# Optimization experiments

Hardware: AMD Instinct MI355X
Metric: run time of the kernel (lower is better)

The kernel has to match this reference:

```python
import jax, jax.numpy as jnp
import numpy as np

C = 512
K = 3
DIL = 1
EPS = 1e-6


def weight_quant(w):
    # BitNet b1.58 ternary quantization with straight-through estimator:
    # scale = mean(|w|); w_q = clamp(round(w/scale), -1, 1) * scale
    s = jnp.maximum(jnp.mean(jnp.abs(w)), 1e-5)
    q = jnp.clip(jnp.round(w / s), -1.0, 1.0) * s
    return w + jax.lax.stop_gradient(q - w)


def conv1d(x, w, b, padding, dilation):
    # x: [B, C, L], w: [O, I, K]
    y = jax.lax.conv_general_dilated(
        x, w, window_strides=(1,), padding=[(padding, padding)],
        rhs_dilation=(dilation,), dimension_numbers=("NCH", "OIH", "NCH"))
    return y + b[None, :, None]


def setup_inputs() -> dict:
    key = jax.random.key(0)
    k0, k1, k2, k3, k4 = jax.random.split(key, 5)
    fan_in = C * K
    lim = 1.0 / np.sqrt(fan_in)
    x = jax.random.normal(k0, (16, C, 4096), dtype=jnp.float32)
    w1 = jax.random.uniform(k1, (C, C, K), jnp.float32, -lim, lim)
    b1 = jax.random.uniform(k2, (C,), jnp.float32, -lim, lim)
    w2 = jax.random.uniform(k3, (C, C, K), jnp.float32, -lim, lim)
    b2 = jax.random.uniform(k4, (C,), jnp.float32, -lim, lim)
    g = jnp.ones((C,), dtype=jnp.float32)  # RMSNorm gain
    return {"x": x, "w1": w1, "b1": b1, "w2": w2, "b2": b2, "g": g}


def reference(x, w1, b1, w2, b2, g):
    residual = x
    # RMSNorm over channel axis (original transposes to [B,L,C], norms last dim)
    ms = jnp.mean(jnp.square(x), axis=1, keepdims=True)
    h = x * jax.lax.rsqrt(ms + EPS) * g[None, :, None]
    h = jax.nn.silu(h)
    p1 = (K * DIL - DIL) // 2
    h = conv1d(h, weight_quant(w1), b1, p1, DIL)
    h = jax.nn.silu(h)
    h = conv1d(h, weight_quant(w2), b2, K // 2, 1)
    return h + residual
```

## Files before the change

### kernel.cpp

```cpp
#include <hip/hip_runtime.h>

#define BATCH 16
#define CCH 512
#define LEN 4096
#define LPAD 4098

typedef unsigned short u16;
typedef __bf16 bf16x8 __attribute__((ext_vector_type(8)));
typedef float f32x4 __attribute__((ext_vector_type(4)));
typedef u16 u16x8 __attribute__((ext_vector_type(8)));
typedef u16 u16x4 __attribute__((ext_vector_type(4)));

__device__ __forceinline__ u16 f2bf(float f) {
    unsigned u = __float_as_uint(f);
    u = (u + 0x7fffu + ((u >> 16) & 1u)) >> 16;
    return (u16)u;
}
__device__ __forceinline__ float bf2f(u16 v) {
    return __uint_as_float(((unsigned)v) << 16);
}
__device__ __forceinline__ float silu_f(float v) {
    return v / (1.f + __expf(-v));
}
__device__ __forceinline__ void async16(const u16* g, u16* l) {
    __builtin_amdgcn_global_load_lds(
        (const __attribute__((address_space(1))) unsigned int*)g,
        (__attribute__((address_space(3))) unsigned int*)l, 16, 0, 0);
}

#define SBAR() __builtin_amdgcn_sched_barrier(0)
#define HWBAR() { SBAR(); __builtin_amdgcn_s_barrier(); SBAR(); }
#define WAIT_LGKM0() { asm volatile("s_waitcnt lgkmcnt(0)" ::: "memory"); SBAR(); }
#define WAIT_VM(n) { asm volatile("s_waitcnt vmcnt(" #n ")" ::: "memory"); SBAR(); }

__global__ __launch_bounds__(256)
void absmean_partial(const float* __restrict__ w1, const float* __restrict__ w2,
                     float* __restrict__ part) {
    const int tid = threadIdx.x;
    const int base = blockIdx.x * 3072;
    float s1 = 0.f, s2 = 0.f;
    for (int i = tid; i < 3072; i += 256) {
        s1 += fabsf(w1[base + i]);
        s2 += fabsf(w2[base + i]);
    }
    __shared__ float r1[256], r2[256];
    r1[tid] = s1; r2[tid] = s2;
    __syncthreads();
    for (int off = 128; off > 0; off >>= 1) {
        if (tid < off) { r1[tid] += r1[tid + off]; r2[tid] += r2[tid + off]; }
        __syncthreads();
    }
    if (tid == 0) { part[blockIdx.x] = r1[0]; part[256 + blockIdx.x] = r2[0]; }
}

__global__ __launch_bounds__(256)
void finalize_scale(const float* __restrict__ part, float* __restrict__ sv) {
    const int tid = threadIdx.x;
    __shared__ float r1[256], r2[256];
    r1[tid] = part[tid]; r2[tid] = part[256 + tid];
    __syncthreads();
    for (int off = 128; off > 0; off >>= 1) {
        if (tid < off) { r1[tid] += r1[tid + off]; r2[tid] += r2[tid + off]; }
        __syncthreads();
    }
    if (tid == 0) {
        sv[0] = fmaxf(r1[0] * (1.f / 786432.f), 1e-5f);
        sv[1] = fmaxf(r2[0] * (1.f / 786432.f), 1e-5f);
    }
}

__global__ __launch_bounds__(256)
void quantize_w(const float* __restrict__ w, const float* __restrict__ sv,
                int sidx, u16* __restrict__ wqt) {
    const int idx = blockIdx.x * 256 + threadIdx.x;
    const float s = sv[sidx];
    float q = rintf(w[idx] / s);
    q = fmaxf(-1.f, fminf(1.f, q));
    const int o   = idx / 1536;
    const int rem = idx - o * 1536;
    const int i   = rem / 3;
    const int k   = rem - i * 3;
    wqt[k * (CCH * CCH) + o * CCH + i] = f2bf(q);
}

__global__ __launch_bounds__(256)
void zero_pads(u16* __restrict__ h, u16* __restrict__ h1) {
    const int idx = blockIdx.x * 256 + threadIdx.x;
    const int b = idx >> 10;
    const int r = (idx >> 9) & 1;
    const int i = idx & 511;
    const size_t off = ((size_t)b * LPAD + (r ? (LPAD - 1) : 0)) * CCH + i;
    h[off] = 0;
    h1[off] = 0;
}

__global__ __launch_bounds__(256)
void rms_silu_transpose(const float* __restrict__ x, const float* __restrict__ g,
                        u16* __restrict__ h_t) {
    __shared__ u16   xt[CCH][33];
    __shared__ float red[8][32];
    __shared__ float rinv[32];
    const int tid = threadIdx.x;
    const int bb  = blockIdx.x >> 7;
    const int l0  = (blockIdx.x & 127) << 5;

    const size_t xbase = (size_t)bb * CCH * LEN + l0;
    {
        const int i_hi = tid >> 3;
        const int l4   = (tid & 7) << 2;
        #pragma unroll
        for (int it = 0; it < 16; ++it) {
            const int i = it * 32 + i_hi;
            const float4 v = *(const float4*)&x[xbase + (size_t)i * LEN + l4];
            xt[i][l4 + 0] = f2bf(v.x);
            xt[i][l4 + 1] = f2bf(v.y);
            xt[i][l4 + 2] = f2bf(v.z);
            xt[i][l4 + 3] = f2bf(v.w);
        }
    }
    __syncthreads();
    {
        const int l = tid & 31, seg = tid >> 5;
        const int ibeg = seg * 64;
        float ss = 0.f;
        #pragma unroll 8
        for (int i = ibeg; i < ibeg + 64; ++i) {
            const float v = bf2f(xt[i][l]);
            ss += v * v;
        }
        red[seg][l] = ss;
    }
    __syncthreads();
    if (tid < 32) {
        float tot = 0.f;
        #pragma unroll
        for (int k2 = 0; k2 < 8; ++k2) tot += red[k2][tid];
        rinv[tid] = rsqrtf(tot * (1.f / 512.f) + 1e-6f);
    }
    __syncthreads();
    {
        const int l  = tid >> 3;
        const int i0 = (tid & 7) << 6;
        const float ri = rinv[l];
        const size_t ob = ((size_t)bb * LPAD + l0 + l + 1) * CCH + i0;
        for (int ii = 0; ii < 64; ii += 8) {
            u16x8 ov;
            #pragma unroll
            for (int jj = 0; jj < 8; ++jj) {
                const int i = i0 + ii + jj;
                float v = bf2f(xt[i][l]) * ri * g[i];
                ov[jj] = f2bf(silu_f(v));
            }
            *(u16x8*)&h_t[ob + ii] = ov;
        }
    }
}

template<int EPI>
__global__ __launch_bounds__(512)
void conv_gemm8(const u16* __restrict__ Bsrc, const u16* __restrict__ Wq,
                const float* __restrict__ sptr, const float* __restrict__ bias,
                const float* __restrict__ resid, u16* __restrict__ outb,
                float* __restrict__ outf) {
    extern __shared__ u16 lds[];
    const int tid  = threadIdx.x;
    const int lane = tid & 63;
    const int wave = tid >> 6;
    const int wm = wave >> 2;
    const int wn = wave & 3;

    const int wgid = (blockIdx.x & 7) * 64 + (blockIdx.x >> 3);
    const int mt = wgid & 1;
    const int nt = wgid >> 1;
    const int o0 = mt << 8;
    const int bb = nt >> 4;
    const int l0 = (nt & 15) << 8;

    const int sr  = tid >> 3;
    const int scu = ((tid & 7) << 3) ^ ((sr & 7) << 3);
    const int sdst = tid << 3;

    const u16* aSrcBase = Wq + (size_t)o0 * CCH + scu;
    const u16* bSrcBase = Bsrc + ((size_t)bb * LPAD + l0) * CCH + scu;

    auto stage = [&](int pb, int T, int h, int ks2, int i02) {
        #pragma unroll
        for (int j = 0; j < 2; ++j) {
            const int r = h * 128 + j * 64 + sr;
            const u16* src = (T == 0)
                ? aSrcBase + ks2 * (CCH * CCH) + r * CCH + i02
                : bSrcBase + (size_t)(r + ks2) * CCH + i02;
            async16(src, &lds[pb * 32768 + T * 16384 + h * 8192 + j * 4096 + sdst]);
        }
    };
    auto stage_full = [&](int pb, int ks2, int i02) {
        stage(pb, 0, 0, ks2, i02);
        stage(pb, 0, 1, ks2, i02);
        stage(pb, 1, 0, ks2, i02);
        stage(pb, 1, 1, ks2, i02);
    };

    const int swz = (lane & 7) << 3;
    const int c0 = ((lane >> 4) << 3) ^ swz;
    const int c1 = (((lane >> 4) << 3) + 32) ^ swz;
    const int aB = wm * 8192 + (lane & 15) * 64;
    const int bB = 16384 + (wn >> 1) * 8192 + ((wn & 1) * 64 + (lane & 15)) * 64;

    bf16x8 ar[4][2], br[4][2];
    f32x4 acc[8][4];
    #pragma unroll
    for (int m = 0; m < 8; ++m)
        #pragma unroll
        for (int n = 0; n < 4; ++n)
            acc[m][n] = (f32x4){0.f, 0.f, 0.f, 0.f};

    auto rdA = [&](int cbuf, int mh) {
        #pragma unroll
        for (int mm = 0; mm < 4; ++mm) {
            const int base = cbuf * 32768 + aB + (mh * 4 + mm) * 1024;
            ar[mm][0] = *(const bf16x8*)&lds[base + c0];
            ar[mm][1] = *(const bf16x8*)&lds[base + c1];
        }
    };
    auto rdB = [&](int cbuf, int nh) {
        #pragma unroll
        for (int nn = 0; nn < 2; ++nn) {
            const int fn = nh * 2 + nn;
            const int base = cbuf * 32768 + bB + fn * 1024;
            br[fn][0] = *(const bf16x8*)&lds[base + c0];
            br[fn][1] = *(const bf16x8*)&lds[base + c1];
        }
    };
    auto mfma16 = [&](int mh, int nh) {
        __builtin_amdgcn_s_setprio(1);
        #pragma unroll
        for (int kk = 0; kk < 2; ++kk)
            #pragma unroll
            for (int mm = 0; mm < 4; ++mm)
                #pragma unroll
                for (int nn = 0; nn < 2; ++nn)
                    acc[mh * 4 + mm][nh * 2 + nn] =
                        __builtin_amdgcn_mfma_f32_16x16x32_bf16(
                            ar[mm][kk], br[nh * 2 + nn][kk],
                            acc[mh * 4 + mm][nh * 2 + nn], 0, 0, 0);
        __builtin_amdgcn_s_setprio(0);
    };

    stage_full(0, 0, 0);
    WAIT_VM(0);
    HWBAR();

    for (int t = 0; t < 24; ++t) {
        const int cur = t & 1;
        if (t + 1 < 24) {
            const int tn = t + 1;
            stage_full(cur ^ 1, tn % 3, (tn / 3) << 6);
        }
        rdB(cur, 0); rdB(cur, 1);
        rdA(cur, 0);
        mfma16(0, 0); mfma16(0, 1);
        rdA(cur, 1);
        mfma16(1, 1); mfma16(1, 0);
        WAIT_LGKM0();
        WAIT_VM(0);
        HWBAR();
    }

    const float sc = sptr[0];

    if (EPI == 1) {
        #pragma unroll
        for (int m = 0; m < 8; ++m) {
            const int o_loc = wm * 128 + m * 16 + ((lane >> 4) << 2);
            const int ob = o0 + o_loc;
            const float b0 = bias[ob + 0], b1 = bias[ob + 1];
            const float b2 = bias[ob + 2], b3 = bias[ob + 3];
            #pragma unroll
            for (int n = 0; n < 4; ++n) {
                const int l_loc = wn * 64 + n * 16 + (lane & 15);
                const f32x4 a = acc[m][n];
                u16x4 ov;
                ov[0] = f2bf(silu_f(sc * a[0] + b0));
                ov[1] = f2bf(silu_f(sc * a[1] + b1));
                ov[2] = f2bf(silu_f(sc * a[2] + b2));
                ov[3] = f2bf(silu_f(sc * a[3] + b3));
                char* p = (char*)lds + l_loc * 512 +
                          (((unsigned)(o_loc << 1)) ^ ((l_loc & 7) << 4));
                *(u16x4*)p = ov;
            }
        }
        __syncthreads();
        const int l_r = tid >> 2;
        const int oq  = (tid & 3) << 3;
        #pragma unroll
        for (int pass = 0; pass < 2; ++pass) {
            const int lr = l_r + pass * 128;
            u16* gdst = outb + ((size_t)bb * LPAD + l0 + lr + 1) * CCH + o0 + oq;
            char* srp = (char*)lds + lr * 512;
            const int swz2 = (lr & 7) << 4;
            #pragma unroll
            for (int c = 0; c < 8; ++c) {
                const uint4 v = *(const uint4*)(srp + (((oq << 1) + c * 64) ^ swz2));
                *(uint4*)(gdst + c * 32) = v;
            }
        }
    } else {
        const int lbase = l0 + wn * 64 + (lane & 15);
        const int obase = o0 + wm * 128 + ((lane >> 4) << 2);
        #pragma unroll
        for (int m = 0; m < 8; ++m) {
            const int ob = obase + m * 16;
            #pragma unroll
            for (int n = 0; n < 4; ++n) {
                const int l = lbase + n * 16;
                const f32x4 a = acc[m][n];
                #pragma unroll
                for (int jj = 0; jj < 4; ++jj) {
                    const size_t idx = ((size_t)bb * CCH + (ob + jj)) * LEN + l;
                    outf[idx] = sc * a[jj] + bias[ob + jj] + resid[idx];
                }
            }
        }
    }
}

extern "C" void kernel_launch(void* const* d_in, const int* in_sizes, int n_in,
                              void* d_out, int out_size, void* d_ws, size_t ws_size,
                              hipStream_t stream) {
    const float* x  = (const float*)d_in[0];
    const float* w1 = (const float*)d_in[1];
    const float* b1 = (const float*)d_in[2];
    const float* w2 = (const float*)d_in[3];
    const float* b2 = (const float*)d_in[4];
    const float* g  = (const float*)d_in[5];
    float* out = (float*)d_out;

    char* ws = (char*)d_ws;
    float* sv   = (float*)ws;
    float* part = (float*)(ws + 256);
    u16* wq1   = (u16*)(ws + 4096);
    u16* wq2   = (u16*)(ws + 4096 + 1572864);
    u16* h_t   = (u16*)(ws + 4096 + 2 * 1572864);
    u16* h1_t  = (u16*)(ws + 4096 + 2 * 1572864 + 67141632);

    hipFuncSetAttribute((const void*)conv_gemm8<1>,
                        hipFuncAttributeMaxDynamicSharedMemorySize, 131072);
    hipFuncSetAttribute((const void*)conv_gemm8<2>,
                        hipFuncAttributeMaxDynamicSharedMemorySize, 131072);

    absmean_partial<<<dim3(256), dim3(256), 0, stream>>>(w1, w2, part);
    finalize_scale<<<dim3(1), dim3(256), 0, stream>>>(part, sv);
    quantize_w<<<dim3(3072), dim3(256), 0, stream>>>(w1, sv, 0, wq1);
    quantize_w<<<dim3(3072), dim3(256), 0, stream>>>(w2, sv, 1, wq2);
    zero_pads<<<dim3(64), dim3(256), 0, stream>>>(h_t, h1_t);
    rms_silu_transpose<<<dim3(2048), dim3(256), 0, stream>>>(x, g, h_t);
    conv_gemm8<1><<<dim3(512), dim3(512), 131072, stream>>>(h_t, wq1, sv, b1,
                                                            nullptr, h1_t, nullptr);
    conv_gemm8<2><<<dim3(512), dim3(512), 131072, stream>>>(h1_t, wq2, sv + 1, b2,
                                                            x, nullptr, out);
}
```

Before: 314.5 us.

## Double threads per GEMM block to 16 waves with smaller per-wave tiles

Raises the conv GEMM workgroup from 8 to 16 waves, giving each wave a 64x64 output tile (4x4 MFMA accumulators) instead of 128x64. Staging is split across twice as many threads, and the epilogue store loop loses one pass. The aim is more latency hiding and lower per-wave register pressure. The cost is more LDS fragment reads per MFMA, because operand reuse per wave drops, plus larger barrier groups.

```diff
diff --git a/kernel.cpp b/kernel.cpp
--- a/kernel.cpp
+++ b/kernel.cpp
@@ -157,7 +157,7 @@
 }
 
 template<int EPI>
-__global__ __launch_bounds__(512)
+__global__ __launch_bounds__(1024)
 void conv_gemm8(const u16* __restrict__ Bsrc, const u16* __restrict__ Wq,
                 const float* __restrict__ sptr, const float* __restrict__ bias,
                 const float* __restrict__ resid, u16* __restrict__ outb,
@@ -183,68 +183,29 @@
     const u16* aSrcBase = Wq + (size_t)o0 * CCH + scu;
     const u16* bSrcBase = Bsrc + ((size_t)bb * LPAD + l0) * CCH + scu;
 
-    auto stage = [&](int pb, int T, int h, int ks2, int i02) {
+    auto stage_full = [&](int pb, int ks2, int i02) {
         #pragma unroll
         for (int j = 0; j < 2; ++j) {
-            const int r = h * 128 + j * 64 + sr;
-            const u16* src = (T == 0)
-                ? aSrcBase + ks2 * (CCH * CCH) + r * CCH + i02
-                : bSrcBase + (size_t)(r + ks2) * CCH + i02;
-            async16(src, &lds[pb * 32768 + T * 16384 + h * 8192 + j * 4096 + sdst]);
-        }
-    };
-    auto stage_full = [&](int pb, int ks2, int i02) {
-        stage(pb, 0, 0, ks2, i02);
-        stage(pb, 0, 1, ks2, i02);
-        stage(pb, 1, 0, ks2, i02);
-        stage(pb, 1, 1, ks2, i02);
+            const int r = j * 128 + sr;
+            async16(aSrcBase + ks2 * (CCH * CCH) + r * CCH + i02,
+                    &lds[pb * 32768 + j * 8192 + sdst]);
+            async16(bSrcBase + (size_t)(r + ks2) * CCH + i02,
+                    &lds[pb * 32768 + 16384 + j * 8192 + sdst]);
+        }
     };
 
     const int swz = (lane & 7) << 3;
     const int c0 = ((lane >> 4) << 3) ^ swz;
     const int c1 = (((lane >> 4) << 3) + 32) ^ swz;
-    const int aB = wm * 8192 + (lane & 15) * 64;
-    const int bB = 16384 + (wn >> 1) * 8192 + ((wn & 1) * 64 + (lane & 15)) * 64;
-
-    bf16x8 ar[4][2], br[4][2];
-    f32x4 acc[8][4];
+    const int aB = wm * 4096 + (lane & 15) * 64;
+    const int bB = 16384 + wn * 4096 + (lane & 15) * 64;
+
+    f32x4 acc[4][4];
     #pragma unroll
-    for (int m = 0; m < 8; ++m)
+    for (int m = 0; m < 4; ++m)
         #pragma unroll
         for (int n = 0; n < 4; ++n)
             acc[m][n] = (f32x4){0.f, 0.f, 0.f, 0.f};
-
-    auto rdA = [&](int cbuf, int mh) {
-        #pragma unroll
-        for (int mm = 0; mm < 4; ++mm) {
-            const int base = cbuf * 32768 + aB + (mh * 4 + mm) * 1024;
-            ar[mm][0] = *(const bf16x8*)&lds[base + c0];
-            ar[mm][1] = *(const bf16x8*)&lds[base + c1];
-        }
-    };
-    auto rdB = [&](int cbuf, int nh) {
-        #pragma unroll
-        for (int nn = 0; nn < 2; ++nn) {
-            const int fn = nh * 2 + nn;
-            const int base = cbuf * 32768 + bB + fn * 1024;
-            br[fn][0] = *(const bf16x8*)&lds[base + c0];
-            br[fn][1] = *(const bf16x8*)&lds[base + c1];
-        }
-    };
-    auto mfma16 = [&](int mh, int nh) {
-        __builtin_amdgcn_s_setprio(1);
-        #pragma unroll
-        for (int kk = 0; kk < 2; ++kk)
-            #pragma unroll
-            for (int mm = 0; mm < 4; ++mm)
-                #pragma unroll
-                for (int nn = 0; nn < 2; ++nn)
-                    acc[mh * 4 + mm][nh * 2 + nn] =
-                        __builtin_amdgcn_mfma_f32_16x16x32_bf16(
-                            ar[mm][kk], br[nh * 2 + nn][kk],
-                            acc[mh * 4 + mm][nh * 2 + nn], 0, 0, 0);
-        __builtin_amdgcn_s_setprio(0);
-    };
 
     stage_full(0, 0, 0);
     WAIT_VM(0);
@@ -252,15 +213,30 @@
 
     for (int t = 0; t < 24; ++t) {
         const int cur = t & 1;
+        const int cbase = cur * 32768;
         if (t + 1 < 24) {
             const int tn = t + 1;
             stage_full(cur ^ 1, tn % 3, (tn / 3) << 6);
         }
-        rdB(cur, 0); rdB(cur, 1);
-        rdA(cur, 0);
-        mfma16(0, 0); mfma16(0, 1);
-        rdA(cur, 1);
-        mfma16(1, 1); mfma16(1, 0);
+        #pragma unroll
+        for (int kk = 0; kk < 2; ++kk) {
+            const int ck = kk ? c1 : c0;
+            bf16x8 ar[4], br[4];
+            #pragma unroll
+            for (int m = 0; m < 4; ++m)
+                ar[m] = *(const bf16x8*)&lds[cbase + aB + m * 1024 + ck];
+            #pragma unroll
+            for (int n = 0; n < 4; ++n)
+                br[n] = *(const bf16x8*)&lds[cbase + bB + n * 1024 + ck];
+            __builtin_amdgcn_s_setprio(1);
+            #pragma unroll
+            for (int m = 0; m < 4; ++m)
+                #pragma unroll
+                for (int n = 0; n < 4; ++n)
+                    acc[m][n] = __builtin_amdgcn_mfma_f32_16x16x32_bf16(
+                        ar[m], br[n], acc[m][n], 0, 0, 0);
+            __builtin_amdgcn_s_setprio(0);
+        }
         WAIT_LGKM0();
         WAIT_VM(0);
         HWBAR();
@@ -270,8 +246,8 @@
 
     if (EPI == 1) {
         #pragma unroll
-        for (int m = 0; m < 8; ++m) {
-            const int o_loc = wm * 128 + m * 16 + ((lane >> 4) << 2);
+        for (int m = 0; m < 4; ++m) {
+            const int o_loc = wm * 64 + m * 16 + ((lane >> 4) << 2);
             const int ob = o0 + o_loc;
             const float b0 = bias[ob + 0], b1 = bias[ob + 1];
             const float b2 = bias[ob + 2], b3 = bias[ob + 3];
@@ -292,23 +268,19 @@
         __syncthreads();
         const int l_r = tid >> 2;
         const int oq  = (tid & 3) << 3;
-        #pragma unroll
-        for (int pass = 0; pass < 2; ++pass) {
-            const int lr = l_r + pass * 128;
-            u16* gdst = outb + ((size_t)bb * LPAD + l0 + lr + 1) * CCH + o0 + oq;
-            char* srp = (char*)lds + lr * 512;
-            const int swz2 = (lr & 7) << 4;
-            #pragma unroll
-            for (int c = 0; c < 8; ++c) {
-                const uint4 v = *(const uint4*)(srp + (((oq << 1) + c * 64) ^ swz2));
-                *(uint4*)(gdst + c * 32) = v;
-            }
+        u16* gdst = outb + ((size_t)bb * LPAD + l0 + l_r + 1) * CCH + o0 + oq;
+        char* srp = (char*)lds + l_r * 512;
+        const int swz2 = (l_r & 7) << 4;
+        #pragma unroll
+        for (int c = 0; c < 8; ++c) {
+            const uint4 v = *(const uint4*)(srp + (((oq << 1) + c * 64) ^ swz2));
+            *(uint4*)(gdst + c * 32) = v;
         }
     } else {
         const int lbase = l0 + wn * 64 + (lane & 15);
-        const int obase = o0 + wm * 128 + ((lane >> 4) << 2);
-        #pragma unroll
-        for (int m = 0; m < 8; ++m) {
+        const int obase = o0 + wm * 64 + ((lane >> 4) << 2);
+        #pragma unroll
+        for (int m = 0; m < 4; ++m) {
             const int ob = obase + m * 16;
             #pragma unroll
             for (int n = 0; n < 4; ++n) {
@@ -354,8 +326,8 @@
     quantize_w<<<dim3(3072), dim3(256), 0, stream>>>(w2, sv, 1, wq2);
     zero_pads<<<dim3(64), dim3(256), 0, stream>>>(h_t, h1_t);
     rms_silu_transpose<<<dim3(2048), dim3(256), 0, stream>>>(x, g, h_t);
-    conv_gemm8<1><<<dim3(512), dim3(512), 131072, stream>>>(h_t, wq1, sv, b1,
-                                                            nullptr, h1_t, nullptr);
-    conv_gemm8<2><<<dim3(512), dim3(512), 131072, stream>>>(h1_t, wq2, sv + 1, b2,
-                                                            x, nullptr, out);
-}
+    conv_gemm8<1><<<dim3(512), dim3(1024), 131072, stream>>>(h_t, wq1, sv, b1,
+                                                             nullptr, h1_t, nullptr);
+    conv_gemm8<2><<<dim3(512), dim3(1024), 131072, stream>>>(h1_t, wq2, sv + 1, b2,
+                                                             x, nullptr, out);
+}
```

Result: faster. 306.9 us (-2.4%).
